# Optimization experiments

Measured on AMD Instinct MI355X. Metric: run time of the kernel, lower is better.

The kernel has to match this reference:

```python
import jax, jax.numpy as jnp
import numpy as np

HIDDEN = 2048
CONNECTIVITY = 0.1
NNZ = int(HIDDEN * HIDDEN * CONNECTIVITY)  # 419430
BATCH, SEQ = 4, 2048


def setup_inputs() -> dict:
    key = jax.random.key(0)
    k1, k2, k3, k4 = jax.random.split(key, 4)
    x_current = jax.random.normal(k1, (BATCH, SEQ, HIDDEN), dtype=jnp.float32)
    x_prev = jax.random.normal(k2, (BATCH, SEQ, HIDDEN), dtype=jnp.float32)
    connection_indices = jax.random.randint(k3, (2, NNZ), 0, HIDDEN, dtype=jnp.int32)
    connection_values = jax.random.normal(k4, (NNZ,), dtype=jnp.float32) * 0.001
    alpha = jnp.float32(0.01)
    return {
        "x_current": x_current,
        "x_prev": x_prev,
        "alpha": alpha,
        "connection_values": connection_values,
        "connection_indices": connection_indices,
    }


def reference(x_current, x_prev, alpha, connection_values, connection_indices):
    H = x_current.shape[-1]
    # Dense W from COO; duplicates are summed (torch sparse_coo_tensor semantics).
    W = jnp.zeros((H, H), dtype=connection_values.dtype).at[
        connection_indices[0], connection_indices[1]
    ].add(connection_values)
    # lateral = x_prev @ W.T : out[b,s,i] = sum_j x_prev[b,s,j] * W[i,j]
    lateral = jnp.einsum("bsj,ij->bsi", x_prev, W)
    return x_current + alpha * lateral
```

## Files before the change

### kernel.cpp

```cpp
#include <hip/hip_runtime.h>
#include <hip/hip_bf16.h>

#define HIDDEN 2048
#define NT 16
#define LDS_BYTES 49152

typedef __attribute__((ext_vector_type(4)))  float f32x4;
typedef __attribute__((ext_vector_type(16))) float f32x16;
typedef __attribute__((ext_vector_type(4)))  int   i32x4;

#define GLDS(gptr, lptr)                                                       \
    __builtin_amdgcn_global_load_lds(                                          \
        (const __attribute__((address_space(1))) void*)(gptr),                 \
        (__attribute__((address_space(3))) void*)(lptr), 16, 0, 0)

#define SCHED0() __builtin_amdgcn_sched_barrier(0)
#define BARRIER() __builtin_amdgcn_s_barrier()
#define LGKMC(n) do { asm volatile("s_waitcnt lgkmcnt(" #n ")" ::: "memory"); SCHED0(); } while (0)
#define VMCNT(n)  do { asm volatile("s_waitcnt vmcnt(" #n ")" ::: "memory"); SCHED0(); } while (0)
#define PRIO1() __builtin_amdgcn_s_setprio(1)
#define PRIO0() __builtin_amdgcn_s_setprio(0)

#define SCALE1 0x7F7F7F7F

#define EXT8(x) __builtin_shufflevector((x), (i32x4){0, 0, 0, 0}, 0, 1, 2, 3, 4, 5, 6, 7)
#define MFMA32(a, b, c)                                                        \
    __builtin_amdgcn_mfma_scale_f32_32x32x64_f8f6f4(                           \
        EXT8(a), EXT8(b), (c), 4, 4, 0, SCALE1, 0, SCALE1)

__device__ __forceinline__ unsigned q_e2m1(float x) {
    float v = fabsf(x);
    unsigned n;
    if      (v < 0.25f) n = 0;
    else if (v < 0.75f) n = 1;
    else if (v < 1.25f) n = 2;
    else if (v < 1.75f) n = 3;
    else if (v < 2.5f)  n = 4;
    else if (v < 3.5f)  n = 5;
    else if (v < 5.0f)  n = 6;
    else                n = 7;
    return n | (x < 0.0f ? 8u : 0u);
}

__device__ __forceinline__ unsigned pack8_e2m1(const f32x4& a, const f32x4& b,
                                               float scale) {
    unsigned w = 0;
    #pragma unroll
    for (int k = 0; k < 4; ++k) {
        w |= q_e2m1(a[k] * scale) << (4 * k);
        w |= q_e2m1(b[k] * scale) << (16 + 4 * k);
    }
    return w;
}

__global__ void scatter_conv_kernel(const float* __restrict__ vals,
                                    const int* __restrict__ rows,
                                    const int* __restrict__ cols,
                                    float* __restrict__ W, int nnz,
                                    const float* __restrict__ xp,
                                    unsigned int* __restrict__ xp4, int n8xp) {
    const int stride = gridDim.x * blockDim.x;
    const int i = blockIdx.x * blockDim.x + threadIdx.x;
    for (int k = i; k < nnz; k += stride)
        atomicAdd(&W[(size_t)rows[k] * HIDDEN + cols[k]], vals[k]);
    for (int j = i; j < n8xp; j += stride) {
        f32x4 a = ((const f32x4*)xp)[2 * j];
        f32x4 b = ((const f32x4*)xp)[2 * j + 1];
        xp4[j] = pack8_e2m1(a, b, 1.0f);
    }
}

__global__ void convw_kernel(const float* __restrict__ W,
                             unsigned int* __restrict__ W4, int n8) {
    const int stride = gridDim.x * blockDim.x;
    for (int j = blockIdx.x * blockDim.x + threadIdx.x; j < n8; j += stride) {
        f32x4 a = ((const f32x4*)W)[2 * j];
        f32x4 b = ((const f32x4*)W)[2 * j + 1];
        W4[j] = pack8_e2m1(a, b, 1024.0f);
    }
}

__global__ __launch_bounds__(256, 3) void gemm_kernel(
    const float* __restrict__ xc,
    const unsigned char* __restrict__ xp4,
    const unsigned char* __restrict__ w4,
    const float* __restrict__ alpha_p,
    float* __restrict__ out)
{
    extern __shared__ __align__(16) char lds[];

    const int tid  = threadIdx.x;
    const int lane = tid & 63;
    const int wave = tid >> 6;
    const int l31  = lane & 31;
    const int kh   = lane >> 5;

    const int xcd = blockIdx.x & 7;
    const int loc = blockIdx.x >> 3;
    const int m0  = (xcd * 8 + (loc >> 4)) * 128;
    const int n0  = (loc & 15) * 128;

    const int wm = (wave >> 1) * 64;
    const int wn = (wave & 1) * 64;

    const int r  = tid >> 2;
    const int rm = r & 31;
    const int sw = (tid & 3) ^ ((rm >> 1) & 3) ^ ((rm >> 3) & 3);
    const unsigned char* const gA = xp4 + (size_t)(m0 + r) * 1024 + sw * 16;
    const unsigned char* const gB = w4  + (size_t)(n0 + r) * 1024 + sw * 16;

#define STAGE(t, buf)                                                          \
    do {                                                                       \
        const size_t _o = (size_t)(t) * 64;                                    \
        char* const _dA = lds + (buf) * 16384 + tid * 16;                      \
        char* const _dB = _dA + 8192;                                          \
        GLDS(gA + _o,             _dA);                                        \
        GLDS(gA + _o + 64 * 1024, _dA + 4096);               \
        GLDS(gB + _o,             _dB);                                        \
        GLDS(gB + _o + 64 * 1024, _dB + 4096);                                 \
    } while (0)

    const int swzr = ((l31 >> 1) & 3) ^ ((l31 >> 3) & 3);
    const int kx0  = ((0 + kh) ^ swzr) * 16;
    const int kx1  = ((2 + kh) ^ swzr) * 16;

    f32x16 acc[2][2] = {};
    i32x4 a0[2], b0[2], a1[2], b1[2];

    STAGE(0, 0);
    STAGE(1, 1);
    VMCNT(4);
    SCHED0(); BARRIER(); SCHED0();

    int cur = 0, stg = 2;

    for (int tt = 0; tt < NT; ++tt) {
        const char* const Ab = lds + cur * 16384 + (wm + l31) * 64;
        const char* const Bb = lds + cur * 16384 + 8192 + (wn + l31) * 64;

        if (tt + 2 < NT) STAGE(tt + 2, stg);
        SCHED0();

        #pragma unroll
        for (int mi = 0; mi < 2; ++mi)
            a0[mi] = *(const i32x4*)(Ab + mi * 2048 + kx0);
        #pragma unroll
        for (int nj = 0; nj < 2; ++nj)
            b0[nj] = *(const i32x4*)(Bb + nj * 2048 + kx0);
        SCHED0();
        #pragma unroll
        for (int mi = 0; mi < 2; ++mi)
            a1[mi] = *(const i32x4*)(Ab + mi * 2048 + kx1);
        #pragma unroll
        for (int nj = 0; nj < 2; ++nj)
            b1[nj] = *(const i32x4*)(Bb + nj * 2048 + kx1);
        SCHED0();
        LGKMC(4);

        PRIO1();
        #pragma unroll
        for (int mi = 0; mi < 2; ++mi)
            #pragma unroll
            for (int nj = 0; nj < 2; ++nj)
                acc[mi][nj] = MFMA32(a0[mi], b0[nj], acc[mi][nj]);
        PRIO0();
        SCHED0();
        LGKMC(0);

        PRIO1();
        #pragma unroll
        for (int mi = 0; mi < 2; ++mi)
            #pragma unroll
            for (int nj = 0; nj < 2; ++nj)
                acc[mi][nj] = MFMA32(a1[mi], b1[nj], acc[mi][nj]);
        PRIO0();
        SCHED0();

        if (tt < NT - 2) { VMCNT(4); } else { VMCNT(0); }
        BARRIER(); SCHED0();

        cur = (cur == 2) ? 0 : cur + 1;
        stg = (stg == 2) ? 0 : stg + 1;
    }

    const float alpha = alpha_p[0] * (1.0f / 1024.0f);
    #pragma unroll
    for (int mi = 0; mi < 2; ++mi) {
        #pragma unroll
        for (int rr = 0; rr < 16; ++rr) {
            const int m = m0 + wm + mi * 32 + (rr & 3) + 8 * (rr >> 2) + 4 * kh;
            #pragma unroll
            for (int nj = 0; nj < 2; ++nj) {
                const int n = n0 + wn + nj * 32 + l31;
                const size_t o = (size_t)m * HIDDEN + n;
                __builtin_nontemporal_store(xc[o] + alpha * acc[mi][nj][rr], &out[o]);
            }
        }
    }
#undef STAGE
}

extern "C" void kernel_launch(void* const* d_in, const int* in_sizes, int n_in,
                              void* d_out, int out_size, void* d_ws, size_t ws_size,
                              hipStream_t stream) {
    const float* xc    = (const float*)d_in[0];
    const float* xp    = (const float*)d_in[1];
    const float* alpha = (const float*)d_in[2];
    const float* vals  = (const float*)d_in[3];
    const int*   idx   = (const int*)d_in[4];
    float* out = (float*)d_out;

    float*         W   = (float*)d_ws;
    unsigned char* W4  = (unsigned char*)((char*)d_ws + (16 << 20));
    unsigned char* xp4 = (unsigned char*)((char*)d_ws + (18 << 20));

    const int nnz = in_sizes[3];
    const int M   = in_sizes[0] / HIDDEN;

    (void)hipFuncSetAttribute((const void*)gemm_kernel,
                              hipFuncAttributeMaxDynamicSharedMemorySize, LDS_BYTES);

    hipMemsetAsync(W, 0, (size_t)HIDDEN * HIDDEN * sizeof(float), stream);
    scatter_conv_kernel<<<2048, 256, 0, stream>>>(vals, idx, idx + nnz, W, nnz,
                                                  xp, (unsigned int*)xp4,
                                                  in_sizes[1] / 8);
    convw_kernel<<<1024, 256, 0, stream>>>(W, (unsigned int*)W4, (HIDDEN * HIDDEN) / 8);

    dim3 grid((M / 128) * 16);
    gemm_kernel<<<grid, 256, LDS_BYTES, stream>>>(xc, xp4, W4, alpha, out);
}
```

Measured before the change: 79.91 us.

## Give each wave private LDS double buffers and drop workgroup barriers in GEMM

Each wave now loads its own 64-row slices of A and B into a private double-buffered LDS region. It issues the next stage after its own fragment reads complete, so block-wide s_barrier calls are no longer needed. This removes inter-wave synchronisation stalls, but A and B tiles are now loaded twice per block (each wave pair duplicates data), which doubles global traffic and LDS use. LDS grows to 64KB and the launch bound drops to 2 blocks per CU, reducing occupancy.

```diff
diff --git a/kernel.cpp b/kernel.cpp
--- a/kernel.cpp
+++ b/kernel.cpp
@@ -3,7 +3,7 @@
 
 #define HIDDEN 2048
 #define NT 16
-#define LDS_BYTES 49152
+#define LDS_BYTES 65536
 
 typedef __attribute__((ext_vector_type(4)))  float f32x4;
 typedef __attribute__((ext_vector_type(16))) float f32x16;
@@ -15,7 +15,6 @@
         (__attribute__((address_space(3))) void*)(lptr), 16, 0, 0)
 
 #define SCHED0() __builtin_amdgcn_sched_barrier(0)
-#define BARRIER() __builtin_amdgcn_s_barrier()
 #define LGKMC(n) do { asm volatile("s_waitcnt lgkmcnt(" #n ")" ::: "memory"); SCHED0(); } while (0)
 #define VMCNT(n)  do { asm volatile("s_waitcnt vmcnt(" #n ")" ::: "memory"); SCHED0(); } while (0)
 #define PRIO1() __builtin_amdgcn_s_setprio(1)
@@ -80,7 +79,7 @@
     }
 }
 
-__global__ __launch_bounds__(256, 3) void gemm_kernel(
+__global__ __launch_bounds__(256, 2) void gemm_kernel(
     const float* __restrict__ xc,
     const unsigned char* __restrict__ xp4,
     const unsigned char* __restrict__ w4,
@@ -103,43 +102,47 @@
     const int wm = (wave >> 1) * 64;
     const int wn = (wave & 1) * 64;
 
-    const int r  = tid >> 2;
-    const int rm = r & 31;
-    const int sw = (tid & 3) ^ ((rm >> 1) & 3) ^ ((rm >> 3) & 3);
-    const unsigned char* const gA = xp4 + (size_t)(m0 + r) * 1024 + sw * 16;
-    const unsigned char* const gB = w4  + (size_t)(n0 + r) * 1024 + sw * 16;
+    const int lr  = lane >> 2;
+    const int bsw = ((lr >> 1) & 3) ^ ((lr >> 3) & 3);
+    const int swE = (lane & 3) ^ bsw;
+    const int swO = swE ^ 2;
+    const unsigned char* const gAe = xp4 + (size_t)(m0 + wm + lr) * 1024 + swE * 16;
+    const unsigned char* const gAo = xp4 + (size_t)(m0 + wm + lr) * 1024 + swO * 16;
+    const unsigned char* const gBe = w4  + (size_t)(n0 + wn + lr) * 1024 + swE * 16;
+    const unsigned char* const gBo = w4  + (size_t)(n0 + wn + lr) * 1024 + swO * 16;
+
+    char* const myLds = lds + wave * 16384;
 
 #define STAGE(t, buf)                                                          \
     do {                                                                       \
         const size_t _o = (size_t)(t) * 64;                                    \
-        char* const _dA = lds + (buf) * 16384 + tid * 16;                      \
-        char* const _dB = _dA + 8192;                                          \
-        GLDS(gA + _o,             _dA);                                        \
-        GLDS(gA + _o + 64 * 1024, _dA + 4096);               \
-        GLDS(gB + _o,             _dB);                                        \
-        GLDS(gB + _o + 64 * 1024, _dB + 4096);                                 \
+        char* const _dA = myLds + (buf) * 8192 + lane * 16;                    \
+        char* const _dB = _dA + 4096;                                          \
+        GLDS(gAe + _o,         _dA);                                           \
+        GLDS(gAo + _o + 16384, _dA + 1024);                      \
+        GLDS(gAe + _o + 32768, _dA + 2048);                      \
+        GLDS(gAo + _o + 49152, _dA + 3072);                      \
+        GLDS(gBe + _o,         _dB);                                           \
+        GLDS(gBo + _o + 16384, _dB + 1024);                                    \
+        GLDS(gBe + _o + 32768, _dB + 2048);                                    \
+        GLDS(gBo + _o + 49152, _dB + 3072);                                    \
     } while (0)
 
     const int swzr = ((l31 >> 1) & 3) ^ ((l31 >> 3) & 3);
     const int kx0  = ((0 + kh) ^ swzr) * 16;
     const int kx1  = ((2 + kh) ^ swzr) * 16;
+    const int rowb = l31 * 64;
 
     f32x16 acc[2][2] = {};
     i32x4 a0[2], b0[2], a1[2], b1[2];
 
     STAGE(0, 0);
     STAGE(1, 1);
-    VMCNT(4);
-    SCHED0(); BARRIER(); SCHED0();
-
-    int cur = 0, stg = 2;
+    VMCNT(8);
 
     for (int tt = 0; tt < NT; ++tt) {
-        const char* const Ab = lds + cur * 16384 + (wm + l31) * 64;
-        const char* const Bb = lds + cur * 16384 + 8192 + (wn + l31) * 64;
-
-        if (tt + 2 < NT) STAGE(tt + 2, stg);
-        SCHED0();
+        const char* const Ab = myLds + (tt & 1) * 8192 + rowb;
+        const char* const Bb = Ab + 4096;
 
         #pragma unroll
         for (int mi = 0; mi < 2; ++mi)
@@ -167,6 +170,9 @@
         SCHED0();
         LGKMC(0);
 
+        if (tt + 2 < NT) STAGE(tt + 2, tt & 1);
+        SCHED0();
+
         PRIO1();
         #pragma unroll
         for (int mi = 0; mi < 2; ++mi)
@@ -176,11 +182,7 @@
         PRIO0();
         SCHED0();
 
-        if (tt < NT - 2) { VMCNT(4); } else { VMCNT(0); }
-        BARRIER(); SCHED0();
-
-        cur = (cur == 2) ? 0 : cur + 1;
-        stg = (stg == 2) ? 0 : stg + 1;
+        if (tt < NT - 2) { VMCNT(8); } else { VMCNT(0); }
     }
 
     const float alpha = alpha_p[0] * (1.0f / 1024.0f);
```

After: 85.85 us. +7.4%, slower.
